# Performance work log

Hardware: AMD Instinct MI355X
Metric: run time of the kernel (lower is better)

## Reference

```python
import jax, jax.numpy as jnp
import numpy as np

B, T, CIN, HID, OUT, H, W = 8, 8, 128, 64, 64, 32, 32


def _conv(x, w, b):
    # x: [B, C, H, W], w: [O, C, kh, kw] -> SAME-padded conv, stride 1
    y = jax.lax.conv_general_dilated(x, w, (1, 1), "SAME",
                                     dimension_numbers=("NCHW", "OIHW", "NCHW"))
    return y + b[None, :, None, None]


def _layer_dir(xs, w_ih, w_hh, b_ih, b_hh, reverse):
    # xs: [T, B, C, H, W]; one direction of a ConvLSTM layer; returns hs [T, B, HID, H, W]
    b, hh_, ww_ = xs.shape[1], xs.shape[3], xs.shape[4]
    h0 = jnp.zeros((b, HID, hh_, ww_), xs.dtype)

    def step(carry, x):
        h, c = carry
        gates = _conv(x, w_ih, b_ih) + _conv(h, w_hh, b_hh)  # [B, 4*HID, H, W]
        i, f, g, o = jnp.split(gates, 4, axis=1)
        c = jax.nn.sigmoid(f) * c + jax.nn.sigmoid(i) * jnp.tanh(g)
        h = jax.nn.sigmoid(o) * jnp.tanh(c)
        return (h, c), h

    _, hs = jax.lax.scan(step, (h0, h0), xs, reverse=reverse)
    return hs


def _forward(features, w_ih0f, w_hh0f, b_ih0f, b_hh0f,
             w_ih0r, w_hh0r, b_ih0r, b_hh0r,
             w_ih1f, w_hh1f, b_ih1f, b_hh1f,
             w_ih1r, w_hh1r, b_ih1r, b_hh1r,
             w_out, b_out):
    xs = jnp.transpose(features, (1, 0, 2, 3, 4))  # [T, B, C, H, W]
    # layer 0, both directions (scan reverse=True aligns outputs to original time order)
    hf = _layer_dir(xs, w_ih0f, w_hh0f, b_ih0f, b_hh0f, False)
    hr = _layer_dir(xs, w_ih0r, w_hh0r, b_ih0r, b_hh0r, True)
    xs1 = jnp.concatenate([hf, hr], axis=2)  # [T, B, 2*HID, H, W] (dropout is identity at eval)
    # layer 1
    hf1 = _layer_dir(xs1, w_ih1f, w_hh1f, b_ih1f, b_hh1f, False)
    hr1 = _layer_dir(xs1, w_ih1r, w_hh1r, b_ih1r, b_hh1r, True)
    last = jnp.concatenate([hf1[-1], hr1[-1]], axis=1)  # output[:, -1] -> [B, 2*HID, H, W]
    return jax.nn.relu(_conv(last, w_out, b_out))


def setup_inputs() -> dict:
    key = jax.random.key(0)
    ks = jax.random.split(key, 24)
    G = 4 * HID
    p = lambda k, s: jax.random.normal(k, s, jnp.float32) * 0.05
    d = {"features": jax.random.normal(ks[0], (B, T, CIN, H, W), jnp.float32)}
    i = 1
    for l, cin in ((0, CIN), (1, 2 * HID)):
        for dr in ("f", "r"):
            d[f"w_ih{l}{dr}"] = p(ks[i], (G, cin, 3, 3)); i += 1
            d[f"w_hh{l}{dr}"] = p(ks[i], (G, HID, 3, 3)); i += 1
            d[f"b_ih{l}{dr}"] = p(ks[i], (G,)); i += 1
            d[f"b_hh{l}{dr}"] = p(ks[i], (G,)); i += 1
    d["w_out"] = p(ks[i], (OUT, 2 * HID, 1, 1)); i += 1
    d["b_out"] = p(ks[i], (OUT,))
    return d


def reference(features, w_ih0f, w_hh0f, b_ih0f, b_hh0f,
              w_ih0r, w_hh0r, b_ih0r, b_hh0r,
              w_ih1f, w_hh1f, b_ih1f, b_hh1f,
              w_ih1r, w_hh1r, b_ih1r, b_hh1r,
              w_out, b_out):
    return _forward(features, w_ih0f, w_hh0f, b_ih0f, b_hh0f,
                    w_ih0r, w_hh0r, b_ih0r, b_hh0r,
                    w_ih1f, w_hh1f, b_ih1f, b_hh1f,
                    w_ih1r, w_hh1r, b_ih1r, b_hh1r,
                    w_out, b_out)
```

## Files before the change

### kernel.cpp

```cpp
#include <hip/hip_runtime.h>
#include <math.h>
#include <stdint.h>


typedef __attribute__((ext_vector_type(8))) short short8;
typedef __attribute__((ext_vector_type(4))) float float4v;

namespace {
constexpr int IMG = 34 * 34 * 64;
constexpr size_t SLOTI = 16ull * IMG;
constexpr int ROWB = 34 * 128;
constexpr int PADB = 8192;
}
template <int N> struct IC { static constexpr int v = N; };

__device__ __forceinline__ uint16_t bf16_rne(float x) {
  uint32_t u = __builtin_bit_cast(uint32_t, x);
  return (uint16_t)((u + 0x7FFFu + ((u >> 16) & 1u)) >> 16);
}
__device__ __forceinline__ float bf16_to_f(uint16_t h) {
  uint32_t u = ((uint32_t)h) << 16;
  return __builtin_bit_cast(float, u);
}

__device__ __forceinline__ void gl_lds16(const void* g, void* l) {
  __builtin_amdgcn_global_load_lds(
      (const __attribute__((address_space(1))) void*)g,
      (__attribute__((address_space(3))) void*)l, 16, 0, 0);
}

__global__ void pack_features(const float* __restrict__ f, uint16_t* __restrict__ out) {
  const size_t i = (size_t)blockIdx.x * 256 + threadIdx.x;
  const int blk_s = (int)(i & 7);
  size_t pp = i >> 3;
  const int px = (int)(pp % 34); pp /= 34;
  const int yy = (int)(pp % 34); pp /= 34;
  const int cg = (int)(pp & 3);
  const int bt = (int)(pp >> 2);
  const int b = bt & 7, t = bt >> 3;
  const int blk = blk_s ^ (px & 7);
  const int pl = blk >> 2, kg = blk & 3;
  short8 sv;
  if (px == 0 || px == 33 || yy == 0 || yy == 33) {
    #pragma unroll
    for (int j = 0; j < 8; ++j) sv[j] = 0;
  } else {
    const int x = px - 1, y = yy - 1;
    #pragma unroll
    for (int j = 0; j < 8; ++j) {
      const int ch = cg * 32 + kg * 8 + j;
      const float fv = f[(((size_t)b * 8 + t) * 128 + ch) * 1024 + y * 32 + x];
      const uint16_t hi = bf16_rne(fv);
      sv[j] = (short)(pl ? bf16_rne(fv - bf16_to_f(hi)) : hi);
    }
  }
  *(short8*)(out + i * 8) = sv;
}

struct WPackArgs {
  const float* wih[4]; const float* whh[4];
  const float* bih[4]; const float* bhh[4];
  uint32_t* wp; float* bp;
};
__global__ void pack_weights(WPackArgs A) {
  const int combo = blockIdx.y;
  const int idx = blockIdx.x * 256 + threadIdx.x;
  const int q = idx & 4095;
  const int rest = idx >> 12;
  const int nt = rest & 1;
  const int ct = rest >> 1;
  const int tap = ct % 9, cg = ct / 9;
  const int w2 = q & 3;
  const int b8s = (q >> 2) & 7;
  const int hcp = (q >> 5) & 15;
  const int g = (q >> 9) & 3;
  const int pl = (q >> 11) & 1;
  const int b8 = b8s ^ (hcp & 7);
  const int kg = b8 & 3;
  const int hcl = hcp * 2 + (b8 >> 2);
  const int n = g * 64 + nt * 32 + hcl;
  const float* wih = A.wih[combo];
  const float* whh = A.whh[combo];
  uint32_t out = 0;
  #pragma unroll
  for (int e = 0; e < 2; ++e) {
    const int ch = cg * 32 + kg * 8 + w2 * 2 + e;
    const float wv = (ch < 128) ? wih[((size_t)n * 128 + ch) * 9 + tap]
                                : whh[((size_t)n * 64 + (ch - 128)) * 9 + tap];
    const uint16_t hi = bf16_rne(wv);
    const uint16_t v = pl ? bf16_rne(wv - bf16_to_f(hi)) : hi;
    out |= ((uint32_t)v) << (16 * e);
  }
  A.wp[(size_t)combo * 442368 + idx] = out;
  if (idx < 256) A.bp[combo * 256 + idx] = A.bih[combo][idx] + A.bhh[combo][idx];
}

struct StepArgs {
  const uint16_t* in0; const uint16_t* in1; const uint16_t* in2;
  int nc0, nc1, nc2;
  const uint32_t* W;
  const float* bias;
  float* cbuf;
  uint16_t* himg;
  float* hf32;
};

template <int ROWS>
__global__ __launch_bounds__(ROWS * 128, ROWS / 2) void conv_lstm_step(StepArgs A0, StepArgs A1) {
  constexpr int NW = ROWS * 2;
  constexpr int THREADS = NW * 64;
  constexpr int BANDS = 32 / ROWS;
  constexpr int LOGB = (ROWS == 4) ? 3 : 4;
  constexpr int ACH = (ROWS == 4) ? 4 : 5;
  constexpr int ASLOT = ACH * NW * 1024;
  constexpr int WCH = 16384 / (NW * 1024);
  constexpr int CNT0 = WCH;
  constexpr int CNT12 = WCH + ACH;

  extern __shared__ char smem[];
  char* Asm_ = smem;
  char* Wsm_ = smem + 2 * ASLOT;

  const StepArgs a = (blockIdx.z == 0) ? A0 : A1;
  const int bx = blockIdx.x;
  const int nt = bx & 1;
  const int band = (bx >> 1) & (BANDS - 1);
  const int b = bx >> (1 + LOGB);
  const int y0 = band * ROWS;
  const int tid = threadIdx.x;
  const int lane = tid & 63;
  const int w = tid >> 6;
  const int m15 = lane & 15;
  const int kg = lane >> 4;
  const int r = w & (ROWS - 1);
  const int hcg = (ROWS == 4) ? (w >> 2) : (w >> 1);

  int offA[2][3][2];
  #pragma unroll
  for (int xh = 0; xh < 2; ++xh)
    #pragma unroll
    for (int kx = 0; kx < 3; ++kx)
      #pragma unroll
      for (int pl = 0; pl < 2; ++pl) {
        const int px = xh * 16 + kx + m15;
        const int sw = (pl * 4 + kg) ^ (px & 7);
        offA[xh][kx][pl] = r * ROWB + px * 128 + sw * 16;
      }
  int offW[2][4];
  {
    const int hcp = hcg * 8 + (m15 >> 1);
    const int b8 = kg + 4 * (m15 & 1);
    #pragma unroll
    for (int pl = 0; pl < 2; ++pl)
      #pragma unroll
      for (int g = 0; g < 4; ++g)
        offW[pl][g] = (((pl * 4 + g) * 16 + hcp) * 8 + (b8 ^ (hcp & 7))) * 16;
  }

  const int ncg = a.nc0 + a.nc1 + a.nc2;
  auto abase = [&](int cg) -> const char* {
    const uint16_t* t;
    if (cg < a.nc0) t = a.in0 + ((size_t)b * a.nc0 + cg) * IMG;
    else if (cg < a.nc0 + a.nc1) t = a.in1 + ((size_t)b * a.nc1 + (cg - a.nc0)) * IMG;
    else t = a.in2 + ((size_t)b * a.nc2 + (cg - a.nc0 - a.nc1)) * IMG;
    return (const char*)t + (size_t)y0 * ROWB;
  };
  auto stageA = [&](int cgi, int par) {
    const char* g = abase(cgi);
    char* d = Asm_ + par * ASLOT;
    #pragma unroll
    for (int j = 0; j < ACH; ++j)
      gl_lds16(g + (size_t)(ACH * w + j) * 1024 + lane * 16, d + (ACH * w + j) * 1024);
  };
  const char* const wbeg = (const char*)a.W + (size_t)nt * 16384;
  const char* const wend = (const char*)a.W + (size_t)ncg * 9 * 32768;
  const char* wsrc = wbeg;
  auto stageW = [&](int slot) {
    char* d = Wsm_ + slot * 16384;
    #pragma unroll
    for (int j = 0; j < WCH; ++j)
      gl_lds16(wsrc + (size_t)(WCH * w + j) * 1024 + lane * 16, d + (WCH * w + j) * 1024);
    wsrc += 32768;
    if (wsrc >= wend) wsrc = wbeg;
  };

  float4v acc[2][4];
  #pragma unroll
  for (int xh = 0; xh < 2; ++xh)
    #pragma unroll
    for (int g = 0; g < 4; ++g) acc[xh][g] = (float4v){0.f, 0.f, 0.f, 0.f};

  stageA(0, 0);
  stageW(0);
  stageW(1);

  for (int cg = 0; cg < ncg; ++cg) {
    auto tap_body = [&](auto tapc) {
      constexpr int TAP = decltype(tapc)::v;
      constexpr int CNT = (TAP == 1 || TAP == 2) ? CNT12 : CNT0;
      constexpr int SLOT2 = (TAP + 2) % 3;
      constexpr int SLOTR = TAP % 3;
      asm volatile("s_waitcnt vmcnt(%0)\n\ts_barrier" :: "n"(CNT) : "memory");
      stageW(SLOT2);
      if (TAP == 0) {
        const int nx = (cg + 1 < ncg) ? cg + 1 : 0;
        stageA(nx, (cg + 1) & 1);
      }
      constexpr int ky = TAP / 3, kx = TAP % 3;
      const char* Ab = Asm_ + (cg & 1) * ASLOT + ky * ROWB;
      const char* Wb = Wsm_ + SLOTR * 16384;
      short8 af[2][2];
      #pragma unroll
      for (int xh = 0; xh < 2; ++xh)
        #pragma unroll
        for (int pl = 0; pl < 2; ++pl)
          af[xh][pl] = *(const short8*)(Ab + offA[xh][kx][pl]);
      short8 wfr[2][4];
      #pragma unroll
      for (int pl = 0; pl < 2; ++pl)
        #pragma unroll
        for (int g = 0; g < 4; ++g)
          wfr[pl][g] = *(const short8*)(Wb + offW[pl][g]);
      __builtin_amdgcn_s_setprio(1);
      #pragma unroll
      for (int xh = 0; xh < 2; ++xh)
        #pragma unroll
        for (int g = 0; g < 4; ++g) {
          acc[xh][g] = __builtin_amdgcn_mfma_f32_16x16x32_bf16(af[xh][0], wfr[0][g], acc[xh][g], 0, 0, 0);
          acc[xh][g] = __builtin_amdgcn_mfma_f32_16x16x32_bf16(af[xh][0], wfr[1][g], acc[xh][g], 0, 0, 0);
          acc[xh][g] = __builtin_amdgcn_mfma_f32_16x16x32_bf16(af[xh][1], wfr[0][g], acc[xh][g], 0, 0, 0);
        }
      __builtin_amdgcn_s_setprio(0);
    };
    tap_body(IC<0>{}); tap_body(IC<1>{}); tap_body(IC<2>{});
    tap_body(IC<3>{}); tap_body(IC<4>{}); tap_body(IC<5>{});
    tap_body(IC<6>{}); tap_body(IC<7>{}); tap_body(IC<8>{});
  }
  asm volatile("s_waitcnt vmcnt(0)" ::: "memory");

  const int hcl = hcg * 16 + m15;
  const int hc = nt * 32 + hcl;
  const int y = y0 + r;
  float bi[4];
  #pragma unroll
  for (int g = 0; g < 4; ++g) bi[g] = a.bias[g * 64 + hc];
  float* crow = a.cbuf + ((size_t)(b * 64 + hc)) * 1024 + y * 32;
  float* hrow = a.hf32 ? a.hf32 + ((size_t)(b * 64 + hc)) * 1024 + y * 32 : nullptr;
  uint16_t* hb = a.himg ? a.himg + ((size_t)(b * 2 + nt)) * IMG : nullptr;
  const int kgb = hcl >> 3, jj = hcl & 7;
  #pragma unroll
  for (int xh = 0; xh < 2; ++xh) {
    const int x0 = xh * 16 + kg * 4;
    float4v cv = *(float4v*)(crow + x0);
    float4v cn, hn;
    #pragma unroll
    for (int q = 0; q < 4; ++q) {
      const float ig = 1.f / (1.f + expf(-(acc[xh][0][q] + bi[0])));
      const float fg = 1.f / (1.f + expf(-(acc[xh][1][q] + bi[1])));
      const float gg = tanhf(acc[xh][2][q] + bi[2]);
      const float og = 1.f / (1.f + expf(-(acc[xh][3][q] + bi[3])));
      const float c2 = fg * cv[q] + ig * gg;
      cn[q] = c2;
      hn[q] = og * tanhf(c2);
    }
    *(float4v*)(crow + x0) = cn;
    if (hrow) *(float4v*)(hrow + x0) = hn;
    if (hb) {
      #pragma unroll
      for (int q = 0; q < 4; ++q) {
        const int px = x0 + q + 1;
        const int sw = px & 7;
        const uint16_t hi = bf16_rne(hn[q]);
        const uint16_t lo = bf16_rne(hn[q] - bf16_to_f(hi));
        const size_t p16 = ((size_t)(y + 1) * 34 + px) * 64;
        hb[p16 + (size_t)(kgb ^ sw) * 8 + jj] = hi;
        hb[p16 + (size_t)((4 + kgb) ^ sw) * 8 + jj] = lo;
      }
    }
  }
  if (hb) {
    {
      const int rr = tid >> 7;
      const int hlf = (tid >> 6) & 1;
      const int jx = tid & 63;
      hb[((size_t)(y0 + 1 + rr) * 34 + hlf * 33) * 64 + jx] = 0;
    }
    if (band == 0) for (int i = tid; i < 2176; i += THREADS) hb[i] = 0;
    if (band == BANDS - 1) for (int i = tid; i < 2176; i += THREADS) hb[(size_t)33 * 2176 + i] = 0;
  }
}

__global__ void final_conv(const float* __restrict__ h1f_last, const float* __restrict__ h1r_last,
                           const float* __restrict__ wout, const float* __restrict__ bout,
                           float* __restrict__ out) {
  __shared__ float Ws[16 * 128];
  const int oq = blockIdx.y;
  for (int i = threadIdx.x; i < 16 * 128; i += 256) Ws[i] = wout[oq * 16 * 128 + i];
  __syncthreads();
  const int gp = blockIdx.x * 256 + threadIdx.x;
  const int b = gp >> 10, p = gp & 1023;
  float acc[16];
  #pragma unroll
  for (int o = 0; o < 16; ++o) acc[o] = bout[oq * 16 + o];
  for (int c = 0; c < 128; ++c) {
    const float xv = (c < 64) ? h1f_last[((size_t)b * 64 + c) * 1024 + p]
                              : h1r_last[((size_t)b * 64 + (c - 64)) * 1024 + p];
    #pragma unroll
    for (int o = 0; o < 16; ++o) acc[o] = fmaf(xv, Ws[o * 128 + c], acc[o]);
  }
  #pragma unroll
  for (int o = 0; o < 16; ++o) {
    const float v = acc[o];
    out[((size_t)b * 64 + oq * 16 + o) * 1024 + p] = v > 0.f ? v : 0.f;
  }
}

extern "C" void kernel_launch(void* const* d_in, const int* in_sizes, int n_in,
                              void* d_out, int out_size, void* d_ws, size_t ws_size,
                              hipStream_t stream) {
  char* p = (char*)d_ws;
  uint16_t* featImg = (uint16_t*)p; p += (size_t)8 * 8 * 4 * IMG * 2 + PADB;
  uint32_t* WP = (uint32_t*)p;      p += (size_t)4 * 442368 * 4;
  float* bp = (float*)p;            p += 4096;
  uint16_t* hf0i = (uint16_t*)p;    p += (size_t)9 * SLOTI * 2 + PADB;
  uint16_t* hr0i = (uint16_t*)p;    p += (size_t)9 * SLOTI * 2 + PADB;
  uint16_t* h1fi = (uint16_t*)p;    p += (size_t)2 * SLOTI * 2 + PADB;
  float* c0f = (float*)p;           p += (size_t)4 * 2097152;
  float* c0r = c0f + 524288;
  float* c1f = c0r + 524288;
  float* c1r = c1f + 524288;
  float* h1f8 = (float*)p;          p += 2097152;
  float* h1r8 = (float*)p;          p += 2097152;

  hipMemsetAsync(c0f, 0, (size_t)4 * 2097152, stream);
  hipMemsetAsync(hf0i, 0, (size_t)SLOTI * 2, stream);
  hipMemsetAsync(hr0i + (size_t)8 * SLOTI, 0, (size_t)SLOTI * 2, stream);
  hipMemsetAsync(h1fi, 0, (size_t)SLOTI * 2, stream);

  pack_features<<<dim3(9248), 256, 0, stream>>>((const float*)d_in[0], featImg);

  WPackArgs wa;
  for (int combo = 0; combo < 4; ++combo) {
    const int base = 1 + combo * 4;
    wa.wih[combo] = (const float*)d_in[base];
    wa.whh[combo] = (const float*)d_in[base + 1];
    wa.bih[combo] = (const float*)d_in[base + 2];
    wa.bhh[combo] = (const float*)d_in[base + 3];
  }
  wa.wp = WP; wa.bp = bp;
  pack_weights<<<dim3(1728, 4), 256, 0, stream>>>(wa);

  constexpr int DYN4 = 2 * 32768 + 3 * 16384;
  constexpr int DYN2 = 2 * 20480 + 3 * 16384;
  (void)hipFuncSetAttribute((const void*)(conv_lstm_step<4>),
                            hipFuncAttributeMaxDynamicSharedMemorySize, DYN4);
  (void)hipFuncSetAttribute((const void*)(conv_lstm_step<2>),
                            hipFuncAttributeMaxDynamicSharedMemorySize, DYN2);

  auto mk = [&](const uint16_t* i0, int n0, const uint16_t* i1, int n1,
                const uint16_t* i2, int n2, int combo, float* cb,
                uint16_t* himg, float* hf32) {
    StepArgs s;
    s.in0 = i0; s.in1 = i1; s.in2 = i2;
    s.nc0 = n0; s.nc1 = n1; s.nc2 = n2;
    s.W = WP + (size_t)combo * 442368; s.bias = bp + combo * 256;
    s.cbuf = cb; s.himg = himg; s.hf32 = hf32;
    return s;
  };

  for (int k = 0; k < 8; ++k) {
    const int tr = 7 - k;
    StepArgs f = mk(featImg + (size_t)k * 8 * 4 * IMG, 4,
                    hf0i + (size_t)k * SLOTI, 2, nullptr, 0,
                    0, c0f, hf0i + (size_t)(k + 1) * SLOTI, nullptr);
    StepArgs r = mk(featImg + (size_t)tr * 8 * 4 * IMG, 4,
                    hr0i + (size_t)(tr + 1) * SLOTI, 2, nullptr, 0,
                    1, c0r, hr0i + (size_t)tr * SLOTI, nullptr);
    conv_lstm_step<4><<<dim3(128, 1, 2), 512, DYN4, stream>>>(f, r);
  }

  for (int t = 0; t < 8; ++t) {
    uint16_t* himg = (t < 7) ? h1fi + (size_t)((t + 1) & 1) * SLOTI : nullptr;
    float* hf32 = (t == 7) ? h1f8 : nullptr;
    StepArgs s = mk(hf0i + (size_t)(t + 1) * SLOTI, 2, hr0i + (size_t)t * SLOTI, 2,
                    h1fi + (size_t)(t & 1) * SLOTI, 2, 2, c1f, himg, hf32);
    if (t == 0) {
      StepArgs rv = mk(hf0i + (size_t)8 * SLOTI, 2, hr0i + (size_t)7 * SLOTI, 2,
                       nullptr, 0, 3, c1r, nullptr, h1r8);
      conv_lstm_step<4><<<dim3(128, 1, 2), 512, DYN4, stream>>>(s, rv);
    } else {
      conv_lstm_step<2><<<dim3(256, 1, 1), 256, DYN2, stream>>>(s, s);
    }
  }

  final_conv<<<dim3(32, 4), 256, 0, stream>>>(
      h1f8, h1r8, (const float*)d_in[17], (const float*)d_in[18], (float*)d_out);
}
```

Baseline: 708.4 us.

## Precompute layer-1 input gate convolutions in one batched kernel before recurrence

Layer 1's input-to-hidden convolution depends only on layer-0 outputs, so it is now computed for all timesteps, plus the reverse direction's single step, in one parallel kernel that writes fp32 gate pre-activations to a workspace. The recurrent step kernels then only convolve the hidden state and add the stored gates, which shortens the serial chain. The first timestep of each recurrence skips the zero hidden-state convolution, which also removes several memsets. The cost is an extra large fp32 workspace and the global reads of precomputed gates in every step's epilogue.

```diff
diff --git a/kernel.cpp b/kernel.cpp
--- a/kernel.cpp
+++ b/kernel.cpp
@@ -11,6 +11,8 @@
 constexpr size_t SLOTI = 16ull * IMG;
 constexpr int ROWB = 34 * 128;
 constexpr int PADB = 8192;
+constexpr size_t GSLOT = 8ull * 256 * 1024;
+constexpr int CGU32 = 73728;
 }
 template <int N> struct IC { static constexpr int v = N; };
 
@@ -100,6 +102,7 @@
   int nc0, nc1, nc2;
   const uint32_t* W;
   const float* bias;
+  const float* gpre;
   float* cbuf;
   uint16_t* himg;
   float* hf32;
@@ -173,7 +176,7 @@
       gl_lds16(g + (size_t)(ACH * w + j) * 1024 + lane * 16, d + (ACH * w + j) * 1024);
   };
   const char* const wbeg = (const char*)a.W + (size_t)nt * 16384;
-  const char* const wend = (const char*)a.W + (size_t)ncg * 9 * 32768;
+  const char* const wend = (const char*)a.W + (size_t)(ncg > 0 ? ncg : 1) * 9 * 32768;
   const char* wsrc = wbeg;
   auto stageW = [&](int slot) {
     char* d = Wsm_ + slot * 16384;
@@ -190,11 +193,207 @@
     #pragma unroll
     for (int g = 0; g < 4; ++g) acc[xh][g] = (float4v){0.f, 0.f, 0.f, 0.f};
 
+  if (ncg > 0) {
+    stageA(0, 0);
+    stageW(0);
+    stageW(1);
+
+    for (int cg = 0; cg < ncg; ++cg) {
+      auto tap_body = [&](auto tapc) {
+        constexpr int TAP = decltype(tapc)::v;
+        constexpr int CNT = (TAP == 1 || TAP == 2) ? CNT12 : CNT0;
+        constexpr int SLOT2 = (TAP + 2) % 3;
+        constexpr int SLOTR = TAP % 3;
+        asm volatile("s_waitcnt vmcnt(%0)\n\ts_barrier" :: "n"(CNT) : "memory");
+        stageW(SLOT2);
+        if (TAP == 0) {
+          const int nx = (cg + 1 < ncg) ? cg + 1 : 0;
+          stageA(nx, (cg + 1) & 1);
+        }
+        constexpr int ky = TAP / 3, kx = TAP % 3;
+        const char* Ab = Asm_ + (cg & 1) * ASLOT + ky * ROWB;
+        const char* Wb = Wsm_ + SLOTR * 16384;
+        short8 af[2][2];
+        #pragma unroll
+        for (int xh = 0; xh < 2; ++xh)
+          #pragma unroll
+          for (int pl = 0; pl < 2; ++pl)
+            af[xh][pl] = *(const short8*)(Ab + offA[xh][kx][pl]);
+        short8 wfr[2][4];
+        #pragma unroll
+        for (int pl = 0; pl < 2; ++pl)
+          #pragma unroll
+          for (int g = 0; g < 4; ++g)
+            wfr[pl][g] = *(const short8*)(Wb + offW[pl][g]);
+        __builtin_amdgcn_s_setprio(1);
+        #pragma unroll
+        for (int xh = 0; xh < 2; ++xh)
+          #pragma unroll
+          for (int g = 0; g < 4; ++g) {
+            acc[xh][g] = __builtin_amdgcn_mfma_f32_16x16x32_bf16(af[xh][0], wfr[0][g], acc[xh][g], 0, 0, 0);
+            acc[xh][g] = __builtin_amdgcn_mfma_f32_16x16x32_bf16(af[xh][0], wfr[1][g], acc[xh][g], 0, 0, 0);
+            acc[xh][g] = __builtin_amdgcn_mfma_f32_16x16x32_bf16(af[xh][1], wfr[0][g], acc[xh][g], 0, 0, 0);
+          }
+        __builtin_amdgcn_s_setprio(0);
+      };
+      tap_body(IC<0>{}); tap_body(IC<1>{}); tap_body(IC<2>{});
+      tap_body(IC<3>{}); tap_body(IC<4>{}); tap_body(IC<5>{});
+      tap_body(IC<6>{}); tap_body(IC<7>{}); tap_body(IC<8>{});
+    }
+    asm volatile("s_waitcnt vmcnt(0)" ::: "memory");
+  }
+
+  const int hcl = hcg * 16 + m15;
+  const int hc = nt * 32 + hcl;
+  const int y = y0 + r;
+  float bi[4];
+  #pragma unroll
+  for (int g = 0; g < 4; ++g) bi[g] = a.bias[g * 64 + hc];
+  float* crow = a.cbuf + ((size_t)(b * 64 + hc)) * 1024 + y * 32;
+  float* hrow = a.hf32 ? a.hf32 + ((size_t)(b * 64 + hc)) * 1024 + y * 32 : nullptr;
+  uint16_t* hb = a.himg ? a.himg + ((size_t)(b * 2 + nt)) * IMG : nullptr;
+  const int kgb = hcl >> 3, jj = hcl & 7;
+  #pragma unroll
+  for (int xh = 0; xh < 2; ++xh) {
+    const int x0 = xh * 16 + kg * 4;
+    float4v cv = *(float4v*)(crow + x0);
+    float4v pre[4];
+    if (a.gpre) {
+      #pragma unroll
+      for (int g = 0; g < 4; ++g)
+        pre[g] = *(const float4v*)(a.gpre + ((size_t)(b * 256 + g * 64 + hc)) * 1024 + y * 32 + x0);
+    } else {
+      #pragma unroll
+      for (int g = 0; g < 4; ++g) pre[g] = (float4v){bi[g], bi[g], bi[g], bi[g]};
+    }
+    float4v cn, hn;
+    #pragma unroll
+    for (int q = 0; q < 4; ++q) {
+      const float ig = 1.f / (1.f + expf(-(acc[xh][0][q] + pre[0][q])));
+      const float fg = 1.f / (1.f + expf(-(acc[xh][1][q] + pre[1][q])));
+      const float gg = tanhf(acc[xh][2][q] + pre[2][q]);
+      const float og = 1.f / (1.f + expf(-(acc[xh][3][q] + pre[3][q])));
+      const float c2 = fg * cv[q] + ig * gg;
+      cn[q] = c2;
+      hn[q] = og * tanhf(c2);
+    }
+    *(float4v*)(crow + x0) = cn;
+    if (hrow) *(float4v*)(hrow + x0) = hn;
+    if (hb) {
+      #pragma unroll
+      for (int q = 0; q < 4; ++q) {
+        const int px = x0 + q + 1;
+        const int sw = px & 7;
+        const uint16_t hi = bf16_rne(hn[q]);
+        const uint16_t lo = bf16_rne(hn[q] - bf16_to_f(hi));
+        const size_t p16 = ((size_t)(y + 1) * 34 + px) * 64;
+        hb[p16 + (size_t)(kgb ^ sw) * 8 + jj] = hi;
+        hb[p16 + (size_t)((4 + kgb) ^ sw) * 8 + jj] = lo;
+      }
+    }
+  }
+  if (hb) {
+    {
+      const int rr = tid >> 7;
+      const int hlf = (tid >> 6) & 1;
+      const int jx = tid & 63;
+      hb[((size_t)(y0 + 1 + rr) * 34 + hlf * 33) * 64 + jx] = 0;
+    }
+    if (band == 0) for (int i = tid; i < 2176; i += THREADS) hb[i] = 0;
+    if (band == BANDS - 1) for (int i = tid; i < 2176; i += THREADS) hb[(size_t)33 * 2176 + i] = 0;
+  }
+}
+
+struct PreArgs {
+  const uint16_t* hf0i; const uint16_t* hr0i;
+  const uint32_t* WP; const float* bp; float* gpre;
+};
+__global__ __launch_bounds__(512, 2) void conv_gates_pre(PreArgs P) {
+  constexpr int ACH = 4, ASLOT = 32768, WCH = 2, CNT0 = 2, CNT12 = 6;
+  extern __shared__ char smem[];
+  char* Asm_ = smem;
+  char* Wsm_ = smem + 65536;
+
+  const int slot = blockIdx.y;
+  const uint16_t* in0; const uint16_t* in1; const uint32_t* Wc; const float* bias;
+  if (slot < 8) {
+    in0 = P.hf0i + (size_t)(slot + 1) * SLOTI; in1 = P.hr0i + (size_t)slot * SLOTI;
+    Wc = P.WP + (size_t)2 * 442368; bias = P.bp + 2 * 256;
+  } else {
+    in0 = P.hf0i + (size_t)8 * SLOTI; in1 = P.hr0i + (size_t)7 * SLOTI;
+    Wc = P.WP + (size_t)3 * 442368; bias = P.bp + 3 * 256;
+  }
+
+  const int bx = blockIdx.x;
+  const int nt = bx & 1;
+  const int band = (bx >> 1) & 7;
+  const int b = bx >> 4;
+  const int y0 = band * 4;
+  const int tid = threadIdx.x;
+  const int lane = tid & 63;
+  const int w = tid >> 6;
+  const int m15 = lane & 15;
+  const int kg = lane >> 4;
+  const int r = w & 3;
+  const int hcg = w >> 2;
+
+  int offA[2][3][2];
+  #pragma unroll
+  for (int xh = 0; xh < 2; ++xh)
+    #pragma unroll
+    for (int kx = 0; kx < 3; ++kx)
+      #pragma unroll
+      for (int pl = 0; pl < 2; ++pl) {
+        const int px = xh * 16 + kx + m15;
+        const int sw = (pl * 4 + kg) ^ (px & 7);
+        offA[xh][kx][pl] = r * ROWB + px * 128 + sw * 16;
+      }
+  int offW[2][4];
+  {
+    const int hcp = hcg * 8 + (m15 >> 1);
+    const int b8 = kg + 4 * (m15 & 1);
+    #pragma unroll
+    for (int pl = 0; pl < 2; ++pl)
+      #pragma unroll
+      for (int g = 0; g < 4; ++g)
+        offW[pl][g] = (((pl * 4 + g) * 16 + hcp) * 8 + (b8 ^ (hcp & 7))) * 16;
+  }
+
+  auto abase = [&](int cg) -> const char* {
+    const uint16_t* t = (cg < 2) ? in0 + ((size_t)b * 2 + cg) * IMG
+                                 : in1 + ((size_t)b * 2 + (cg - 2)) * IMG;
+    return (const char*)t + (size_t)y0 * ROWB;
+  };
+  auto stageA = [&](int cgi, int par) {
+    const char* g = abase(cgi);
+    char* d = Asm_ + par * ASLOT;
+    #pragma unroll
+    for (int j = 0; j < ACH; ++j)
+      gl_lds16(g + (size_t)(ACH * w + j) * 1024 + lane * 16, d + (ACH * w + j) * 1024);
+  };
+  const char* const wbeg = (const char*)Wc + (size_t)nt * 16384;
+  const char* const wend = (const char*)Wc + (size_t)4 * 9 * 32768;
+  const char* wsrc = wbeg;
+  auto stageW = [&](int slotw) {
+    char* d = Wsm_ + slotw * 16384;
+    #pragma unroll
+    for (int j = 0; j < WCH; ++j)
+      gl_lds16(wsrc + (size_t)(WCH * w + j) * 1024 + lane * 16, d + (WCH * w + j) * 1024);
+    wsrc += 32768;
+    if (wsrc >= wend) wsrc = wbeg;
+  };
+
+  float4v acc[2][4];
+  #pragma unroll
+  for (int xh = 0; xh < 2; ++xh)
+    #pragma unroll
+    for (int g = 0; g < 4; ++g) acc[xh][g] = (float4v){0.f, 0.f, 0.f, 0.f};
+
   stageA(0, 0);
   stageW(0);
   stageW(1);
 
-  for (int cg = 0; cg < ncg; ++cg) {
+  for (int cg = 0; cg < 4; ++cg) {
     auto tap_body = [&](auto tapc) {
       constexpr int TAP = decltype(tapc)::v;
       constexpr int CNT = (TAP == 1 || TAP == 2) ? CNT12 : CNT0;
@@ -203,7 +402,7 @@
       asm volatile("s_waitcnt vmcnt(%0)\n\ts_barrier" :: "n"(CNT) : "memory");
       stageW(SLOT2);
       if (TAP == 0) {
-        const int nx = (cg + 1 < ncg) ? cg + 1 : 0;
+        const int nx = (cg + 1 < 4) ? cg + 1 : 0;
         stageA(nx, (cg + 1) & 1);
       }
       constexpr int ky = TAP / 3, kx = TAP % 3;
@@ -241,52 +440,18 @@
   const int hcl = hcg * 16 + m15;
   const int hc = nt * 32 + hcl;
   const int y = y0 + r;
-  float bi[4];
-  #pragma unroll
-  for (int g = 0; g < 4; ++g) bi[g] = a.bias[g * 64 + hc];
-  float* crow = a.cbuf + ((size_t)(b * 64 + hc)) * 1024 + y * 32;
-  float* hrow = a.hf32 ? a.hf32 + ((size_t)(b * 64 + hc)) * 1024 + y * 32 : nullptr;
-  uint16_t* hb = a.himg ? a.himg + ((size_t)(b * 2 + nt)) * IMG : nullptr;
-  const int kgb = hcl >> 3, jj = hcl & 7;
+  float* gb = P.gpre + (size_t)slot * GSLOT + (size_t)b * 262144;
   #pragma unroll
   for (int xh = 0; xh < 2; ++xh) {
     const int x0 = xh * 16 + kg * 4;
-    float4v cv = *(float4v*)(crow + x0);
-    float4v cn, hn;
-    #pragma unroll
-    for (int q = 0; q < 4; ++q) {
-      const float ig = 1.f / (1.f + expf(-(acc[xh][0][q] + bi[0])));
-      const float fg = 1.f / (1.f + expf(-(acc[xh][1][q] + bi[1])));
-      const float gg = tanhf(acc[xh][2][q] + bi[2]);
-      const float og = 1.f / (1.f + expf(-(acc[xh][3][q] + bi[3])));
-      const float c2 = fg * cv[q] + ig * gg;
-      cn[q] = c2;
-      hn[q] = og * tanhf(c2);
-    }
-    *(float4v*)(crow + x0) = cn;
-    if (hrow) *(float4v*)(hrow + x0) = hn;
-    if (hb) {
-      #pragma unroll
-      for (int q = 0; q < 4; ++q) {
-        const int px = x0 + q + 1;
-        const int sw = px & 7;
-        const uint16_t hi = bf16_rne(hn[q]);
-        const uint16_t lo = bf16_rne(hn[q] - bf16_to_f(hi));
-        const size_t p16 = ((size_t)(y + 1) * 34 + px) * 64;
-        hb[p16 + (size_t)(kgb ^ sw) * 8 + jj] = hi;
-        hb[p16 + (size_t)((4 + kgb) ^ sw) * 8 + jj] = lo;
-      }
-    }
-  }
-  if (hb) {
-    {
-      const int rr = tid >> 7;
-      const int hlf = (tid >> 6) & 1;
-      const int jx = tid & 63;
-      hb[((size_t)(y0 + 1 + rr) * 34 + hlf * 33) * 64 + jx] = 0;
-    }
-    if (band == 0) for (int i = tid; i < 2176; i += THREADS) hb[i] = 0;
-    if (band == BANDS - 1) for (int i = tid; i < 2176; i += THREADS) hb[(size_t)33 * 2176 + i] = 0;
+    #pragma unroll
+    for (int g = 0; g < 4; ++g) {
+      float4v v = acc[xh][g];
+      const float bv = bias[g * 64 + hc];
+      #pragma unroll
+      for (int q = 0; q < 4; ++q) v[q] += bv;
+      *(float4v*)(gb + ((size_t)(g * 64 + hc)) * 1024 + y * 32 + x0) = v;
+    }
   }
 }
 
@@ -331,11 +496,9 @@
   float* c1r = c1f + 524288;
   float* h1f8 = (float*)p;          p += 2097152;
   float* h1r8 = (float*)p;          p += 2097152;
+  float* gpre = (float*)p;          p += (size_t)9 * GSLOT * 4;
 
   hipMemsetAsync(c0f, 0, (size_t)4 * 2097152, stream);
-  hipMemsetAsync(hf0i, 0, (size_t)SLOTI * 2, stream);
-  hipMemsetAsync(hr0i + (size_t)8 * SLOTI, 0, (size_t)SLOTI * 2, stream);
-  hipMemsetAsync(h1fi, 0, (size_t)SLOTI * 2, stream);
 
   pack_features<<<dim3(9248), 256, 0, stream>>>((const float*)d_in[0], featImg);
 
@@ -356,41 +519,55 @@
                             hipFuncAttributeMaxDynamicSharedMemorySize, DYN4);
   (void)hipFuncSetAttribute((const void*)(conv_lstm_step<2>),
                             hipFuncAttributeMaxDynamicSharedMemorySize, DYN2);
+  (void)hipFuncSetAttribute((const void*)conv_gates_pre,
+                            hipFuncAttributeMaxDynamicSharedMemorySize, DYN4);
 
   auto mk = [&](const uint16_t* i0, int n0, const uint16_t* i1, int n1,
-                const uint16_t* i2, int n2, int combo, float* cb,
-                uint16_t* himg, float* hf32) {
+                const uint16_t* i2, int n2, int combo, int cgskip, float* cb,
+                uint16_t* himg, float* hf32, const float* gp) {
     StepArgs s;
     s.in0 = i0; s.in1 = i1; s.in2 = i2;
     s.nc0 = n0; s.nc1 = n1; s.nc2 = n2;
-    s.W = WP + (size_t)combo * 442368; s.bias = bp + combo * 256;
-    s.cbuf = cb; s.himg = himg; s.hf32 = hf32;
+    s.W = WP + (size_t)combo * 442368 + (size_t)cgskip * CGU32;
+    s.bias = bp + combo * 256;
+    s.gpre = gp; s.cbuf = cb; s.himg = himg; s.hf32 = hf32;
     return s;
   };
 
   for (int k = 0; k < 8; ++k) {
     const int tr = 7 - k;
-    StepArgs f = mk(featImg + (size_t)k * 8 * 4 * IMG, 4,
-                    hf0i + (size_t)k * SLOTI, 2, nullptr, 0,
-                    0, c0f, hf0i + (size_t)(k + 1) * SLOTI, nullptr);
-    StepArgs r = mk(featImg + (size_t)tr * 8 * 4 * IMG, 4,
-                    hr0i + (size_t)(tr + 1) * SLOTI, 2, nullptr, 0,
-                    1, c0r, hr0i + (size_t)tr * SLOTI, nullptr);
+    StepArgs f = (k == 0)
+        ? mk(featImg, 4, nullptr, 0, nullptr, 0,
+             0, 0, c0f, hf0i + (size_t)1 * SLOTI, nullptr, nullptr)
+        : mk(featImg + (size_t)k * 8 * 4 * IMG, 4,
+             hf0i + (size_t)k * SLOTI, 2, nullptr, 0,
+             0, 0, c0f, hf0i + (size_t)(k + 1) * SLOTI, nullptr, nullptr);
+    StepArgs r = (k == 0)
+        ? mk(featImg + (size_t)7 * 8 * 4 * IMG, 4, nullptr, 0, nullptr, 0,
+             1, 0, c0r, hr0i + (size_t)7 * SLOTI, nullptr, nullptr)
+        : mk(featImg + (size_t)tr * 8 * 4 * IMG, 4,
+             hr0i + (size_t)(tr + 1) * SLOTI, 2, nullptr, 0,
+             1, 0, c0r, hr0i + (size_t)tr * SLOTI, nullptr, nullptr);
     conv_lstm_step<4><<<dim3(128, 1, 2), 512, DYN4, stream>>>(f, r);
   }
 
-  for (int t = 0; t < 8; ++t) {
+  PreArgs pa; pa.hf0i = hf0i; pa.hr0i = hr0i; pa.WP = WP; pa.bp = bp; pa.gpre = gpre;
+  conv_gates_pre<<<dim3(128, 9), 512, DYN4, stream>>>(pa);
+
+  {
+    StepArgs f0 = mk(nullptr, 0, nullptr, 0, nullptr, 0,
+                     2, 0, c1f, h1fi + (size_t)1 * SLOTI, nullptr, gpre);
+    StepArgs rv = mk(nullptr, 0, nullptr, 0, nullptr, 0,
+                     3, 0, c1r, nullptr, h1r8, gpre + (size_t)8 * GSLOT);
+    conv_lstm_step<4><<<dim3(128, 1, 2), 512, DYN4, stream>>>(f0, rv);
+  }
+
+  for (int t = 1; t < 8; ++t) {
     uint16_t* himg = (t < 7) ? h1fi + (size_t)((t + 1) & 1) * SLOTI : nullptr;
     float* hf32 = (t == 7) ? h1f8 : nullptr;
-    StepArgs s = mk(hf0i + (size_t)(t + 1) * SLOTI, 2, hr0i + (size_t)t * SLOTI, 2,
-                    h1fi + (size_t)(t & 1) * SLOTI, 2, 2, c1f, himg, hf32);
-    if (t == 0) {
-      StepArgs rv = mk(hf0i + (size_t)8 * SLOTI, 2, hr0i + (size_t)7 * SLOTI, 2,
-                       nullptr, 0, 3, c1r, nullptr, h1r8);
-      conv_lstm_step<4><<<dim3(128, 1, 2), 512, DYN4, stream>>>(s, rv);
-    } else {
-      conv_lstm_step<2><<<dim3(256, 1, 1), 256, DYN2, stream>>>(s, s);
-    }
+    StepArgs s = mk(h1fi + (size_t)(t & 1) * SLOTI, 2, nullptr, 0, nullptr, 0,
+                    2, 4, c1f, himg, hf32, gpre + (size_t)t * GSLOT);
+    conv_lstm_step<2><<<dim3(256, 1, 1), 256, DYN2, stream>>>(s, s);
   }
 
   final_conv<<<dim3(32, 4), 256, 0, stream>>>(
```

Result: no change. 717.4 us (median of 2 runs) (+1.3%).
